# Kernel optimization log

Hardware: AMD Instinct MI355X
Metric: run time of the kernel (lower is better)

The kernel has to match this reference:

```python
import jax, jax.numpy as jnp
import numpy as np

B, T, C, H = 4, 2048, 1024, 16
HS = C // H  # head_size = 64
FF = 4 * C   # 4096
EPS = 1e-5


def _layernorm(x, g, b):
    mu = jnp.mean(x, axis=-1, keepdims=True)
    var = jnp.mean(jnp.square(x - mu), axis=-1, keepdims=True)
    return (x - mu) * jax.lax.rsqrt(var + EPS) * g + b


def setup_inputs() -> dict:
    key = jax.random.key(0)
    ks = jax.random.split(key, 12)
    s_in = 1.0 / np.sqrt(C)
    s_ff = 1.0 / np.sqrt(FF)
    return {
        "x": jax.random.normal(ks[0], (B, T, C), jnp.float32),
        # per-head projection weights stacked: [H, C, HS]
        "Wq": jax.random.normal(ks[1], (H, C, HS), jnp.float32) * s_in,
        "Wk": jax.random.normal(ks[2], (H, C, HS), jnp.float32) * s_in,
        "Wv": jax.random.normal(ks[3], (H, C, HS), jnp.float32) * s_in,
        "Wo": jax.random.normal(ks[4], (C, C), jnp.float32) * s_in,
        "bo": jnp.zeros((C,), jnp.float32),
        "g1": jnp.ones((C,), jnp.float32),
        "b1": jnp.zeros((C,), jnp.float32),
        "g2": jnp.ones((C,), jnp.float32),
        "b2": jnp.zeros((C,), jnp.float32),
        "W1": jax.random.normal(ks[5], (C, FF), jnp.float32) * s_in,
        "bf1": jnp.zeros((FF,), jnp.float32),
        "W2": jax.random.normal(ks[6], (FF, C), jnp.float32) * s_ff,
        "bf2": jnp.zeros((C,), jnp.float32),
    }


def reference(x, Wq, Wk, Wv, Wo, bo, g1, b1, g2, b2, W1, bf1, W2, bf2):
    # pre-norm
    h = _layernorm(x, g1, b1)                       # [B,T,C]
    q = jnp.einsum('btc,hcd->bhtd', h, Wq)          # [B,H,T,HS]
    k = jnp.einsum('btc,hcd->bhtd', h, Wk)
    v = jnp.einsum('btc,hcd->bhtd', h, Wv)
    w = jnp.einsum('bhtd,bhsd->bhts', q, k) * (HS ** -0.5)  # [B,H,T,S]
    mask = jnp.tril(jnp.ones((T, T), bool))          # causal tril
    w = jnp.where(mask[None, None], w, -jnp.inf)
    # NB: original code softmaxes over dim=1 of [B,T,T], i.e. the QUERY axis
    w = jax.nn.softmax(w, axis=-2)
    o = jnp.einsum('bhts,bhsd->bhtd', w, v)          # [B,H,T,HS]
    o = jnp.transpose(o, (0, 2, 1, 3)).reshape(B, T, C)  # concat heads
    x = x + o @ Wo + bo                              # residual 1 (dropout=0)
    f = _layernorm(x, g2, b2)
    ff = jax.nn.relu(f @ W1 + bf1) @ W2 + bf2        # FFN (dropout=0)
    return x + ff
```

## Files before the change

kernel.cpp:

```cpp
#include <hip/hip_runtime.h>


#define T_SEQ 2048
#define SCALE2 0.1803368801f

typedef __attribute__((ext_vector_type(8))) short short8;
typedef __attribute__((ext_vector_type(4))) float f32x4;

typedef __attribute__((address_space(1))) unsigned int g_u32;
typedef __attribute__((address_space(3))) unsigned int l_u32;

__device__ __forceinline__ unsigned short f2bf(float f) {
  union { float f; unsigned u; } x; x.f = f;
  unsigned r = (x.u + 0x7FFFu + ((x.u >> 16) & 1u)) >> 16;
  return (unsigned short)r;
}

__device__ __forceinline__ void g2lds16(const void* g, void* l) {
  __builtin_amdgcn_global_load_lds((g_u32*)g, (l_u32*)l, 16, 0, 0);
}

template <int EPI>
__global__ __launch_bounds__(256) void gemm_bt(
    const unsigned short* __restrict__ A, const unsigned short* __restrict__ Bt,
    int M, int N, int K,
    unsigned short* __restrict__ out16, float* __restrict__ outF,
    const float* __restrict__ bias, const float* __restrict__ resid) {
  __shared__ unsigned short ldsA[128 * 64];
  __shared__ unsigned short ldsB[128 * 64];
  const int tid = threadIdx.x;
  const int lane = tid & 63, wid = tid >> 6;
  const int wm = wid >> 1, wn = wid & 1;
  const int mBase = blockIdx.y * 128, nBase = blockIdx.x * 128;

  f32x4 acc[4][4];
#pragma unroll
  for (int i = 0; i < 4; ++i)
#pragma unroll
    for (int j = 0; j < 4; ++j)
#pragma unroll
      for (int e = 0; e < 4; ++e) acc[i][j][e] = 0.f;

  const int nKT = K >> 6;
  for (int kt = 0; kt < nKT; ++kt) {
    const int k0 = kt << 6;
#pragma unroll
    for (int it = 0; it < 4; ++it) {
      int g = it * 256 + wid * 64 + lane;
      int row = g >> 3, colL = g & 7;
      int col = colL ^ (row & 7);
      g2lds16(A + ((size_t)(mBase + row) * K + k0 + col * 8),
              &ldsA[(it * 256 + wid * 64) * 8]);
      g2lds16(Bt + ((size_t)(nBase + row) * K + k0 + col * 8),
              &ldsB[(it * 256 + wid * 64) * 8]);
    }
    __syncthreads();

    short8 af[4][2], bf[4][2];
#pragma unroll
    for (int fm = 0; fm < 4; ++fm)
#pragma unroll
      for (int ks = 0; ks < 2; ++ks) {
        int r = wm * 64 + fm * 16 + (lane & 15);
        int c = (ks * 4 + (lane >> 4)) ^ (r & 7);
        af[fm][ks] = *(const short8*)&ldsA[r * 64 + c * 8];
      }
#pragma unroll
    for (int fn = 0; fn < 4; ++fn)
#pragma unroll
      for (int ks = 0; ks < 2; ++ks) {
        int r = wn * 64 + fn * 16 + (lane & 15);
        int c = (ks * 4 + (lane >> 4)) ^ (r & 7);
        bf[fn][ks] = *(const short8*)&ldsB[r * 64 + c * 8];
      }
#pragma unroll
    for (int fm = 0; fm < 4; ++fm)
#pragma unroll
      for (int fn = 0; fn < 4; ++fn)
#pragma unroll
        for (int ks = 0; ks < 2; ++ks)
          acc[fm][fn] = __builtin_amdgcn_mfma_f32_16x16x32_bf16(
              af[fm][ks], bf[fn][ks], acc[fm][fn], 0, 0, 0);
    __syncthreads();
  }

#pragma unroll
  for (int fm = 0; fm < 4; ++fm)
#pragma unroll
    for (int fn = 0; fn < 4; ++fn) {
      int col = nBase + wn * 64 + fn * 16 + (lane & 15);
      int row0 = mBase + wm * 64 + fm * 16 + ((lane >> 4) << 2);
      if (EPI == 0) {
#pragma unroll
        for (int r = 0; r < 4; ++r)
          out16[(size_t)(row0 + r) * N + col] = f2bf(acc[fm][fn][r]);
      } else if (EPI == 1) {
        float bv = bias[col];
#pragma unroll
        for (int r = 0; r < 4; ++r) {
          size_t idx = (size_t)(row0 + r) * N + col;
          outF[idx] = acc[fm][fn][r] + bv + resid[idx];
        }
      } else {
        float bv = bias[col];
#pragma unroll
        for (int r = 0; r < 4; ++r)
          out16[(size_t)(row0 + r) * N + col] =
              f2bf(fmaxf(acc[fm][fn][r] + bv, 0.f));
      }
    }
}

__global__ __launch_bounds__(256) void ln_bf16(
    const float* __restrict__ x, const float* __restrict__ gw,
    const float* __restrict__ bw, unsigned short* __restrict__ out) {
  __shared__ float red[8];
  const int row = blockIdx.x, tid = threadIdx.x;
  const float4 v = ((const float4*)(x + (size_t)row * 1024))[tid];
  float s = v.x + v.y + v.z + v.w;
  float q = v.x * v.x + v.y * v.y + v.z * v.z + v.w * v.w;
#pragma unroll
  for (int off = 32; off >= 1; off >>= 1) {
    s += __shfl_down(s, off);
    q += __shfl_down(q, off);
  }
  const int lane = tid & 63, wid = tid >> 6;
  if (lane == 0) { red[wid] = s; red[4 + wid] = q; }
  __syncthreads();
  float S = red[0] + red[1] + red[2] + red[3];
  float Q = red[4] + red[5] + red[6] + red[7];
  float mu = S * (1.f / 1024.f);
  float var = Q * (1.f / 1024.f) - mu * mu;
  float rs = rsqrtf(var + 1e-5f);
  int c = tid * 4;
  ushort4 ov;
  ov.x = f2bf((v.x - mu) * rs * gw[c + 0] + bw[c + 0]);
  ov.y = f2bf((v.y - mu) * rs * gw[c + 1] + bw[c + 1]);
  ov.z = f2bf((v.z - mu) * rs * gw[c + 2] + bw[c + 2]);
  ov.w = f2bf((v.w - mu) * rs * gw[c + 3] + bw[c + 3]);
  *(ushort4*)&out[(size_t)row * 1024 + c] = ov;
}

__global__ __launch_bounds__(256) void pack_qkv(
    const float* __restrict__ Wq, const float* __restrict__ Wk,
    const float* __restrict__ Wv, unsigned short* __restrict__ out) {
  __shared__ float tile[64 * 65];
  const int tid = threadIdx.x;
  const float* W = (blockIdx.z == 0) ? Wq : (blockIdx.z == 1) ? Wk : Wv;
  const int h = blockIdx.y, r0 = blockIdx.x * 64;
#pragma unroll
  for (int it = 0; it < 4; ++it) {
    int e4 = it * 256 + tid;
    int r = e4 >> 4, c4 = e4 & 15;
    float4 v = *(const float4*)&W[((size_t)h * 1024 + r0 + r) * 64 + c4 * 4];
    tile[r * 65 + c4 * 4 + 0] = v.x;
    tile[r * 65 + c4 * 4 + 1] = v.y;
    tile[r * 65 + c4 * 4 + 2] = v.z;
    tile[r * 65 + c4 * 4 + 3] = v.w;
  }
  __syncthreads();
#pragma unroll
  for (int it = 0; it < 4; ++it) {
    int e4 = it * 256 + tid;
    int d = e4 >> 4, r4 = e4 & 15;
    ushort4 ov;
    ov.x = f2bf(tile[(r4 * 4 + 0) * 65 + d]);
    ov.y = f2bf(tile[(r4 * 4 + 1) * 65 + d]);
    ov.z = f2bf(tile[(r4 * 4 + 2) * 65 + d]);
    ov.w = f2bf(tile[(r4 * 4 + 3) * 65 + d]);
    *(ushort4*)&out[(size_t)(blockIdx.z * 1024 + h * 64 + d) * 1024 + r0 +
                    r4 * 4] = ov;
  }
}

__global__ __launch_bounds__(256) void transpose_cast(
    const float* __restrict__ in, unsigned short* __restrict__ out, int R,
    int C) {
  __shared__ float tile[64 * 65];
  const int tid = threadIdx.x;
  const int r0 = blockIdx.x * 64, c0 = blockIdx.y * 64;
#pragma unroll
  for (int it = 0; it < 4; ++it) {
    int e4 = it * 256 + tid;
    int r = e4 >> 4, c4 = e4 & 15;
    float4 v = *(const float4*)&in[(size_t)(r0 + r) * C + c0 + c4 * 4];
    tile[r * 65 + c4 * 4 + 0] = v.x;
    tile[r * 65 + c4 * 4 + 1] = v.y;
    tile[r * 65 + c4 * 4 + 2] = v.z;
    tile[r * 65 + c4 * 4 + 3] = v.w;
  }
  __syncthreads();
#pragma unroll
  for (int it = 0; it < 4; ++it) {
    int e4 = it * 256 + tid;
    int c = e4 >> 4, r4 = e4 & 15;
    ushort4 ov;
    ov.x = f2bf(tile[(r4 * 4 + 0) * 65 + c]);
    ov.y = f2bf(tile[(r4 * 4 + 1) * 65 + c]);
    ov.z = f2bf(tile[(r4 * 4 + 2) * 65 + c]);
    ov.w = f2bf(tile[(r4 * 4 + 3) * 65 + c]);
    *(ushort4*)&out[(size_t)(c0 + c) * R + r0 + r4 * 4] = ov;
  }
}

__global__ __launch_bounds__(256) void vtrans(
    const unsigned short* __restrict__ qkv, unsigned short* __restrict__ vT) {
  __shared__ unsigned short tile[64 * 66];
  const int tid = threadIdx.x;
  const int bh = blockIdx.y, b = bh >> 4, h = bh & 15;
  const int t0 = blockIdx.x * 64;
#pragma unroll
  for (int it = 0; it < 8; ++it) {
    int e2 = it * 256 + tid;
    int r = e2 >> 5, c2 = e2 & 31;
    unsigned v = *(const unsigned*)&qkv[(size_t)(b * T_SEQ + t0 + r) * 3072 +
                                        2048 + h * 64 + c2 * 2];
    *(unsigned*)&tile[r * 66 + c2 * 2] = v;
  }
  __syncthreads();
#pragma unroll
  for (int it = 0; it < 8; ++it) {
    int e2 = it * 256 + tid;
    int d = e2 >> 5, t2 = e2 & 31;
    unsigned short a = tile[(t2 * 2) * 66 + d];
    unsigned short bb = tile[(t2 * 2 + 1) * 66 + d];
    unsigned pk = (unsigned)a | ((unsigned)bb << 16);
    *(unsigned*)&vT[(size_t)(bh * 64 + d) * T_SEQ + t0 + t2 * 2] = pk;
  }
}

__global__ __launch_bounds__(256) void attn_stats(
    const unsigned short* __restrict__ qkv, float* __restrict__ linvOut) {
  __shared__ unsigned short qt[4][2][64 * 64];
  __shared__ float redL[4][2][64];
  const int tid = threadIdx.x, lane = tid & 63, w = tid >> 6;
  const int bh = blockIdx.y, b = bh >> 4, h = bh & 15;
  const int sx = blockIdx.x;
  const int sA = sx * 64, sB = (31 - sx) * 64;
  const int nT = 32 - sx;
  const int bDiag = 31 - 2 * sx;

  short8 kfA[4][2], kfB[4][2];
#pragma unroll
  for (int fn = 0; fn < 4; ++fn)
#pragma unroll
    for (int ks = 0; ks < 2; ++ks) {
      int d = 1024 + h * 64 + ks * 32 + ((lane >> 4) << 3);
      kfA[fn][ks] = *(const short8*)&qkv[(size_t)(b * T_SEQ + sA + fn * 16 +
                                                  (lane & 15)) * 3072 + d];
      kfB[fn][ks] = *(const short8*)&qkv[(size_t)(b * T_SEQ + sB + fn * 16 +
                                                  (lane & 15)) * 3072 + d];
    }
  float lA[4] = {0.f, 0.f, 0.f, 0.f}, lB[4] = {0.f, 0.f, 0.f, 0.f};

  auto stageQ = [&](int buf, int idx) {
    int t0 = sA + idx * 64;
#pragma unroll
    for (int it = 0; it < 8; ++it) {
      int g = it * 64 + lane;
      int row = g >> 3;
      int col = (g & 7) ^ (row & 7);
      g2lds16(qkv + ((size_t)(b * T_SEQ + t0 + row) * 3072 + h * 64 + col * 8),
              &qt[w][buf][it * 512]);
    }
  };

  auto accum = [&](const short8 (&af)[2], const short8 (&kf)[4][2],
                   float (&lacc)[4], int sBase, int t0, int mf, bool diag) {
    f32x4 sc[4];
#pragma unroll
    for (int fn = 0; fn < 4; ++fn)
#pragma unroll
      for (int e = 0; e < 4; ++e) sc[fn][e] = 0.f;
    __builtin_amdgcn_s_setprio(1);
#pragma unroll
    for (int fn = 0; fn < 4; ++fn)
#pragma unroll
      for (int ks = 0; ks < 2; ++ks)
        sc[fn] = __builtin_amdgcn_mfma_f32_16x16x32_bf16(af[ks], kf[fn][ks],
                                                         sc[fn], 0, 0, 0);
    __builtin_amdgcn_s_setprio(0);
    const int tRow = t0 + mf * 16 + ((lane >> 4) << 2);
    if (diag) {
#pragma unroll
      for (int fn = 0; fn < 4; ++fn) {
        int s = sBase + fn * 16 + (lane & 15);
#pragma unroll
        for (int r = 0; r < 4; ++r) {
          float e = exp2f(sc[fn][r] * SCALE2);
          lacc[fn] += (tRow + r >= s) ? e : 0.f;
        }
      }
    } else {
#pragma unroll
      for (int fn = 0; fn < 4; ++fn)
#pragma unroll
        for (int r = 0; r < 4; ++r) lacc[fn] += exp2f(sc[fn][r] * SCALE2);
    }
  };

  int idx = w, cur = 0;
  stageQ(0, idx);
  for (; idx < nT; idx += 4, cur ^= 1) {
    if (idx + 4 < nT) {
      stageQ(cur ^ 1, idx + 4);
      asm volatile("s_waitcnt vmcnt(8)" ::: "memory");
    } else {
      asm volatile("s_waitcnt vmcnt(0)" ::: "memory");
    }
    const int t0 = sA + idx * 64;
    const bool doB = idx >= bDiag;
#pragma unroll
    for (int mf = 0; mf < 4; ++mf) {
      short8 af[2];
#pragma unroll
      for (int ks = 0; ks < 2; ++ks) {
        int r = mf * 16 + (lane & 15);
        int c = (ks * 4 + (lane >> 4)) ^ (r & 7);
        af[ks] = *(const short8*)&qt[w][cur][r * 64 + c * 8];
      }
      accum(af, kfA, lA, sA, t0, mf, idx == 0);
      if (doB) accum(af, kfB, lB, sB, t0, mf, idx == bDiag);
    }
  }
#pragma unroll
  for (int fn = 0; fn < 4; ++fn) {
    lA[fn] += __shfl_down(lA[fn], 32);
    lA[fn] += __shfl_down(lA[fn], 16);
    lB[fn] += __shfl_down(lB[fn], 32);
    lB[fn] += __shfl_down(lB[fn], 16);
  }
  if (lane < 16) {
#pragma unroll
    for (int fn = 0; fn < 4; ++fn) {
      redL[w][0][fn * 16 + lane] = lA[fn];
      redL[w][1][fn * 16 + lane] = lB[fn];
    }
  }
  __syncthreads();
  if (tid < 128) {
    int which = tid >> 6;
    float l = redL[0][which][lane] + redL[1][which][lane] +
              redL[2][which][lane] + redL[3][which][lane];
    int sbase = (which == 0) ? sA : sB;
    linvOut[(size_t)bh * T_SEQ + sbase + lane] = 1.f / l;
  }
}

__global__ __launch_bounds__(256, 2) void attn_pv(
    const unsigned short* __restrict__ qkv, const unsigned short* __restrict__ vT,
    const float* __restrict__ linvIn, unsigned short* __restrict__ o) {
  __shared__ unsigned short kbuf[2][64 * 64];
  __shared__ unsigned short vbuf[2][64 * 64];
  __shared__ unsigned short pl[256 * 64];
  const int tid = threadIdx.x, lane = tid & 63, wid = tid >> 6;
  const int bh = blockIdx.y, b = bh >> 4, h = bh & 15;
  const int bx = blockIdx.x;
  const int tA = bx * 128, tB = (15 - bx) * 128;
  const int nSTA = 2 * bx + 2, nSTB = 32 - 2 * bx;

  short8 qfA[2][2], qfB[2][2];
#pragma unroll
  for (int mf = 0; mf < 2; ++mf)
#pragma unroll
    for (int ks = 0; ks < 2; ++ks) {
      int d = h * 64 + ks * 32 + ((lane >> 4) << 3);
      int rloc = wid * 32 + mf * 16 + (lane & 15);
      qfA[mf][ks] =
          *(const short8*)&qkv[(size_t)(b * T_SEQ + tA + rloc) * 3072 + d];
      qfB[mf][ks] =
          *(const short8*)&qkv[(size_t)(b * T_SEQ + tB + rloc) * 3072 + d];
    }
  f32x4 oaccA[2][4], oaccB[2][4];
#pragma unroll
  for (int i = 0; i < 2; ++i)
#pragma unroll
    for (int j = 0; j < 4; ++j)
#pragma unroll
      for (int e = 0; e < 4; ++e) { oaccA[i][j][e] = 0.f; oaccB[i][j][e] = 0.f; }

  auto stage = [&](int buf, int st) {
#pragma unroll
    for (int it = 0; it < 2; ++it) {
      int g = it * 256 + tid;
      int row = g >> 3, colL = g & 7;
      int col = colL ^ (row & 7);
      g2lds16(qkv + ((size_t)(b * T_SEQ + st * 64 + row) * 3072 + 1024 +
                     h * 64 + col * 8),
              &kbuf[buf][(it * 256 + wid * 64) * 8]);
      g2lds16(vT + ((size_t)(bh * 64 + row) * T_SEQ + st * 64 + col * 8),
              &vbuf[buf][(it * 256 + wid * 64) * 8]);
    }
  };

  auto qkstore = [&](const short8 (&qf)[2][2], int rowBase, int tBase, int s0,
                     float cc, bool maskNeeded, int cur) {
    f32x4 sc[2][4];
#pragma unroll
    for (int i = 0; i < 2; ++i)
#pragma unroll
      for (int j = 0; j < 4; ++j)
#pragma unroll
        for (int e = 0; e < 4; ++e) sc[i][j][e] = 0.f;
    __builtin_amdgcn_s_setprio(1);
#pragma unroll
    for (int fn = 0; fn < 4; ++fn)
#pragma unroll
      for (int ks = 0; ks < 2; ++ks) {
        int r = fn * 16 + (lane & 15);
        int c = (ks * 4 + (lane >> 4)) ^ (r & 7);
        short8 kfr = *(const short8*)&kbuf[cur][r * 64 + c * 8];
        sc[0][fn] = __builtin_amdgcn_mfma_f32_16x16x32_bf16(qf[0][ks], kfr,
                                                            sc[0][fn], 0, 0, 0);
        sc[1][fn] = __builtin_amdgcn_mfma_f32_16x16x32_bf16(qf[1][ks], kfr,
                                                            sc[1][fn], 0, 0, 0);
      }
    __builtin_amdgcn_s_setprio(0);
#pragma unroll
    for (int fn = 0; fn < 4; ++fn) {
      float ccf = __shfl(cc, fn * 16 + (lane & 15));
      int sg = s0 + fn * 16 + (lane & 15);
      int colb = (fn * 16 + (lane & 15)) * 2;
#pragma unroll
      for (int mf = 0; mf < 2; ++mf) {
        int rowB = rowBase + wid * 32 + mf * 16 + ((lane >> 4) << 2);
        int tRow = tBase + wid * 32 + mf * 16 + ((lane >> 4) << 2);
#pragma unroll
        for (int r = 0; r < 4; ++r) {
          float p = exp2f(fmaf(sc[mf][fn][r], SCALE2, ccf));
          if (maskNeeded) p = (tRow + r >= sg) ? p : 0.f;
          int row = rowB + r;
          int byteoff = row * 128 + (colb ^ ((row & 7) << 4));
          *(unsigned short*)((char*)pl + byteoff) = f2bf(p);
        }
      }
    }
  };

  stage(0, 0);
  int cur = 0;
  __syncthreads();

  for (int st = 0; st < nSTB; ++st) {
    const int s0 = st * 64;
    float lv = linvIn[(size_t)bh * T_SEQ + s0 + lane];
    float cc = __log2f(lv);
    const bool doA = st < nSTA;

    if (doA) qkstore(qfA, 0, tA, s0, cc, st >= nSTA - 2, cur);
    qkstore(qfB, 128, tB, s0, cc, st >= nSTB - 2, cur);
    __syncthreads();

    if (st + 1 < nSTB) stage(cur ^ 1, st + 1);

    __builtin_amdgcn_s_setprio(1);
#pragma unroll
    for (int ks = 0; ks < 2; ++ks) {
      short8 paA[2], paB[2];
#pragma unroll
      for (int mf = 0; mf < 2; ++mf) {
        int rowa = wid * 32 + mf * 16 + (lane & 15);
        int kb = ks * 64 + ((lane >> 4) << 4);
        paB[mf] = *(const short8*)((const char*)pl + (128 + rowa) * 128 +
                                   (kb ^ ((rowa & 7) << 4)));
        if (doA)
          paA[mf] = *(const short8*)((const char*)pl + rowa * 128 +
                                     (kb ^ ((rowa & 7) << 4)));
      }
#pragma unroll
      for (int df = 0; df < 4; ++df) {
        int r = df * 16 + (lane & 15);
        int c = (ks * 4 + (lane >> 4)) ^ (r & 7);
        short8 vb = *(const short8*)&vbuf[cur][r * 64 + c * 8];
        oaccB[0][df] = __builtin_amdgcn_mfma_f32_16x16x32_bf16(paB[0], vb,
                                                               oaccB[0][df], 0, 0, 0);
        oaccB[1][df] = __builtin_amdgcn_mfma_f32_16x16x32_bf16(paB[1], vb,
                                                               oaccB[1][df], 0, 0, 0);
        if (doA) {
          oaccA[0][df] = __builtin_amdgcn_mfma_f32_16x16x32_bf16(paA[0], vb,
                                                                 oaccA[0][df], 0, 0, 0);
          oaccA[1][df] = __builtin_amdgcn_mfma_f32_16x16x32_bf16(paA[1], vb,
                                                                 oaccA[1][df], 0, 0, 0);
        }
      }
    }
    __builtin_amdgcn_s_setprio(0);
    __syncthreads();
    cur ^= 1;
  }
#pragma unroll
  for (int mf = 0; mf < 2; ++mf)
#pragma unroll
    for (int df = 0; df < 4; ++df) {
      int d = h * 64 + df * 16 + (lane & 15);
      int ra = tA + wid * 32 + mf * 16 + ((lane >> 4) << 2);
      int rb = tB + wid * 32 + mf * 16 + ((lane >> 4) << 2);
#pragma unroll
      for (int r = 0; r < 4; ++r) {
        o[(size_t)(b * T_SEQ + ra + r) * 1024 + d] = f2bf(oaccA[mf][df][r]);
        o[(size_t)(b * T_SEQ + rb + r) * 1024 + d] = f2bf(oaccB[mf][df][r]);
      }
    }
}

extern "C" void kernel_launch(void* const* d_in, const int* in_sizes, int n_in,
                              void* d_out, int out_size, void* d_ws,
                              size_t ws_size, hipStream_t stream) {
  const float* x = (const float*)d_in[0];
  const float* Wq = (const float*)d_in[1];
  const float* Wk = (const float*)d_in[2];
  const float* Wv = (const float*)d_in[3];
  const float* Wo = (const float*)d_in[4];
  const float* bo = (const float*)d_in[5];
  const float* g1 = (const float*)d_in[6];
  const float* b1 = (const float*)d_in[7];
  const float* g2 = (const float*)d_in[8];
  const float* b2 = (const float*)d_in[9];
  const float* W1 = (const float*)d_in[10];
  const float* bf1 = (const float*)d_in[11];
  const float* W2 = (const float*)d_in[12];
  const float* bf2 = (const float*)d_in[13];
  float* out = (float*)d_out;

  char* ws = (char*)d_ws;
  size_t off = 0;
  auto alloc = [&](size_t bytes) {
    char* p = ws + off;
    off += (bytes + 255) & ~(size_t)255;
    return p;
  };
  unsigned short* Wqkv = (unsigned short*)alloc(3072ull * 1024 * 2);
  unsigned short* WoT = (unsigned short*)alloc(1024ull * 1024 * 2);
  unsigned short* W1T = (unsigned short*)alloc(4096ull * 1024 * 2);
  unsigned short* W2T = (unsigned short*)alloc(1024ull * 4096 * 2);
  unsigned short* hbuf = (unsigned short*)alloc(8192ull * 1024 * 2);
  char* regionE = alloc(8192ull * 3072 * 2 + 64ull * 64 * 2048 * 2);
  unsigned short* qkv = (unsigned short*)regionE;
  unsigned short* vT = (unsigned short*)(regionE + 8192ull * 3072 * 2);
  unsigned short* act = (unsigned short*)regionE;
  float* lbuf = (float*)alloc(64ull * 2048 * 4);
  float* x1 = (float*)alloc(8192ull * 1024 * 4);
  unsigned short* fbuf = (unsigned short*)alloc(8192ull * 1024 * 2);
  unsigned short* obuf = hbuf;

  (void)in_sizes; (void)n_in; (void)out_size; (void)ws_size;

  pack_qkv<<<dim3(16, 16, 3), 256, 0, stream>>>(Wq, Wk, Wv, Wqkv);
  transpose_cast<<<dim3(16, 16), 256, 0, stream>>>(Wo, WoT, 1024, 1024);
  transpose_cast<<<dim3(16, 64), 256, 0, stream>>>(W1, W1T, 1024, 4096);
  transpose_cast<<<dim3(64, 16), 256, 0, stream>>>(W2, W2T, 4096, 1024);
  ln_bf16<<<8192, 256, 0, stream>>>(x, g1, b1, hbuf);
  gemm_bt<0><<<dim3(24, 64), 256, 0, stream>>>(hbuf, Wqkv, 8192, 3072, 1024,
                                               qkv, nullptr, nullptr, nullptr);
  vtrans<<<dim3(32, 64), 256, 0, stream>>>(qkv, vT);
  attn_stats<<<dim3(16, 64), 256, 0, stream>>>(qkv, lbuf);
  attn_pv<<<dim3(8, 64), 256, 0, stream>>>(qkv, vT, lbuf, obuf);
  gemm_bt<1><<<dim3(8, 64), 256, 0, stream>>>(obuf, WoT, 8192, 1024, 1024,
                                              nullptr, x1, bo, x);
  ln_bf16<<<8192, 256, 0, stream>>>(x1, g2, b2, fbuf);
  gemm_bt<2><<<dim3(32, 64), 256, 0, stream>>>(fbuf, W1T, 8192, 4096, 1024, act,
                                               nullptr, bf1, nullptr);
  gemm_bt<1><<<dim3(8, 64), 256, 0, stream>>>(act, W2T, 8192, 1024, 4096,
                                              nullptr, out, bf2, x1);
}
```

Before: 471.7 us.

## Add 256x256 double-buffered GEMM, XCD swizzle, and fold softmax normalizer into V

Introduces a 512-thread 256x256-tile GEMM with double-buffered LDS staging (128KB dynamic shared) for the QKV and FFN1 projections, aiming to raise data reuse and overlap loads with MFMA. It adds an XCD-aware block swizzle and MFMA priority hints to the existing GEMM. It also moves the per-key softmax normalizer (query-axis softmax) into the V transpose by scaling V rows, which removes the per-tile log/shuffle/fma from the attention inner loop. Scaling V before bf16 rounding changes rounding slightly, and the large LDS footprint limits occupancy.

```diff
diff --git a/kernel.cpp b/kernel.cpp
--- a/kernel.cpp
+++ b/kernel.cpp
@@ -15,9 +15,117 @@
   unsigned r = (x.u + 0x7FFFu + ((x.u >> 16) & 1u)) >> 16;
   return (unsigned short)r;
 }
+__device__ __forceinline__ float bf2f(unsigned short u) {
+  union { unsigned u; float f; } x; x.u = (unsigned)u << 16;
+  return x.f;
+}
 
 __device__ __forceinline__ void g2lds16(const void* g, void* l) {
   __builtin_amdgcn_global_load_lds((g_u32*)g, (l_u32*)l, 16, 0, 0);
+}
+
+__device__ __forceinline__ int xcd_swz(int flat, int nwg) {
+  if ((nwg & 7) != 0) return flat;
+  return (flat & 7) * (nwg >> 3) + (flat >> 3);
+}
+
+template <int EPI>
+__global__ __launch_bounds__(512, 2) void gemm256(
+    const unsigned short* __restrict__ A, const unsigned short* __restrict__ Bt,
+    int M, int N, int K,
+    unsigned short* __restrict__ out16, const float* __restrict__ bias) {
+  extern __shared__ unsigned short lds[];
+  unsigned short* ldsA = lds;
+  unsigned short* ldsB = lds + 2 * 16384;
+  const int tid = threadIdx.x, lane = tid & 63, wid = tid >> 6;
+  const int wm = wid >> 2, wn = wid & 3;
+  const int nx = gridDim.x;
+  const int flat = blockIdx.y * nx + blockIdx.x;
+  const int swz = xcd_swz(flat, nx * gridDim.y);
+  const int mBase = (swz / nx) * 256, nBase = (swz % nx) * 256;
+
+  f32x4 acc[8][4];
+#pragma unroll
+  for (int i = 0; i < 8; ++i)
+#pragma unroll
+    for (int j = 0; j < 4; ++j)
+#pragma unroll
+      for (int e = 0; e < 4; ++e) acc[i][j][e] = 0.f;
+
+  auto stage = [&](int buf, int kt) {
+    const int k0 = kt << 6;
+#pragma unroll
+    for (int it = 0; it < 4; ++it) {
+      int g = it * 512 + tid;
+      int row = g >> 3, colL = g & 7;
+      int col = colL ^ (row & 7);
+      g2lds16(A + ((size_t)(mBase + row) * K + k0 + col * 8),
+              &ldsA[buf * 16384 + (it * 512 + wid * 64) * 8]);
+      g2lds16(Bt + ((size_t)(nBase + row) * K + k0 + col * 8),
+              &ldsB[buf * 16384 + (it * 512 + wid * 64) * 8]);
+    }
+  };
+
+  const int nKT = K >> 6;
+  stage(0, 0);
+  __syncthreads();
+  int cur = 0;
+  for (int kt = 0; kt < nKT; ++kt) {
+    if (kt + 1 < nKT) stage(cur ^ 1, kt + 1);
+
+    short8 bf[4][2];
+#pragma unroll
+    for (int fn = 0; fn < 4; ++fn)
+#pragma unroll
+      for (int ks = 0; ks < 2; ++ks) {
+        int r = wn * 64 + fn * 16 + (lane & 15);
+        int c = (ks * 4 + (lane >> 4)) ^ (r & 7);
+        bf[fn][ks] = *(const short8*)&ldsB[cur * 16384 + r * 64 + c * 8];
+      }
+#pragma unroll
+    for (int q = 0; q < 4; ++q) {
+      short8 af[2][2];
+#pragma unroll
+      for (int mf = 0; mf < 2; ++mf)
+#pragma unroll
+        for (int ks = 0; ks < 2; ++ks) {
+          int r = wm * 128 + q * 32 + mf * 16 + (lane & 15);
+          int c = (ks * 4 + (lane >> 4)) ^ (r & 7);
+          af[mf][ks] = *(const short8*)&ldsA[cur * 16384 + r * 64 + c * 8];
+        }
+      __builtin_amdgcn_s_setprio(1);
+#pragma unroll
+      for (int mf = 0; mf < 2; ++mf)
+#pragma unroll
+        for (int fn = 0; fn < 4; ++fn)
+#pragma unroll
+          for (int ks = 0; ks < 2; ++ks)
+            acc[q * 2 + mf][fn] = __builtin_amdgcn_mfma_f32_16x16x32_bf16(
+                af[mf][ks], bf[fn][ks], acc[q * 2 + mf][fn], 0, 0, 0);
+      __builtin_amdgcn_s_setprio(0);
+    }
+    __syncthreads();
+    cur ^= 1;
+  }
+
+#pragma unroll
+  for (int am = 0; am < 8; ++am)
+#pragma unroll
+    for (int fn = 0; fn < 4; ++fn) {
+      int col = nBase + wn * 64 + fn * 16 + (lane & 15);
+      int row0 = mBase + wm * 128 + am * 16 + ((lane >> 4) << 2);
+      if (EPI == 0) {
+#pragma unroll
+        for (int r = 0; r < 4; ++r)
+          out16[(size_t)(row0 + r) * N + col] = f2bf(acc[am][fn][r]);
+      } else {
+        float bv = bias[col];
+#pragma unroll
+        for (int r = 0; r < 4; ++r)
+          out16[(size_t)(row0 + r) * N + col] =
+              f2bf(fmaxf(acc[am][fn][r] + bv, 0.f));
+      }
+    }
 }
 
 template <int EPI>
@@ -31,7 +139,10 @@
   const int tid = threadIdx.x;
   const int lane = tid & 63, wid = tid >> 6;
   const int wm = wid >> 1, wn = wid & 1;
-  const int mBase = blockIdx.y * 128, nBase = blockIdx.x * 128;
+  const int nx = gridDim.x;
+  const int flat = blockIdx.y * nx + blockIdx.x;
+  const int swz = xcd_swz(flat, nx * gridDim.y);
+  const int mBase = (swz / nx) * 128, nBase = (swz % nx) * 128;
 
   f32x4 acc[4][4];
 #pragma unroll
@@ -73,6 +184,7 @@
         int c = (ks * 4 + (lane >> 4)) ^ (r & 7);
         bf[fn][ks] = *(const short8*)&ldsB[r * 64 + c * 8];
       }
+    __builtin_amdgcn_s_setprio(1);
 #pragma unroll
     for (int fm = 0; fm < 4; ++fm)
 #pragma unroll
@@ -81,6 +193,7 @@
         for (int ks = 0; ks < 2; ++ks)
           acc[fm][fn] = __builtin_amdgcn_mfma_f32_16x16x32_bf16(
               af[fm][ks], bf[fn][ks], acc[fm][fn], 0, 0, 0);
+    __builtin_amdgcn_s_setprio(0);
     __syncthreads();
   }
 
@@ -204,7 +317,8 @@
 }
 
 __global__ __launch_bounds__(256) void vtrans(
-    const unsigned short* __restrict__ qkv, unsigned short* __restrict__ vT) {
+    const unsigned short* __restrict__ qkv, const float* __restrict__ linv,
+    unsigned short* __restrict__ vT) {
   __shared__ unsigned short tile[64 * 66];
   const int tid = threadIdx.x;
   const int bh = blockIdx.y, b = bh >> 4, h = bh & 15;
@@ -215,7 +329,10 @@
     int r = e2 >> 5, c2 = e2 & 31;
     unsigned v = *(const unsigned*)&qkv[(size_t)(b * T_SEQ + t0 + r) * 3072 +
                                         2048 + h * 64 + c2 * 2];
-    *(unsigned*)&tile[r * 66 + c2 * 2] = v;
+    float li = linv[(size_t)bh * T_SEQ + t0 + r];
+    unsigned short lo = f2bf(bf2f((unsigned short)(v & 0xffff)) * li);
+    unsigned short hi = f2bf(bf2f((unsigned short)(v >> 16)) * li);
+    *(unsigned*)&tile[r * 66 + c2 * 2] = (unsigned)lo | ((unsigned)hi << 16);
   }
   __syncthreads();
 #pragma unroll
@@ -349,7 +466,7 @@
 
 __global__ __launch_bounds__(256, 2) void attn_pv(
     const unsigned short* __restrict__ qkv, const unsigned short* __restrict__ vT,
-    const float* __restrict__ linvIn, unsigned short* __restrict__ o) {
+    unsigned short* __restrict__ o) {
   __shared__ unsigned short kbuf[2][64 * 64];
   __shared__ unsigned short vbuf[2][64 * 64];
   __shared__ unsigned short pl[256 * 64];
@@ -394,7 +511,7 @@
   };
 
   auto qkstore = [&](const short8 (&qf)[2][2], int rowBase, int tBase, int s0,
-                     float cc, bool maskNeeded, int cur) {
+                     bool maskNeeded, int cur) {
     f32x4 sc[2][4];
 #pragma unroll
     for (int i = 0; i < 2; ++i)
@@ -418,7 +535,6 @@
     __builtin_amdgcn_s_setprio(0);
 #pragma unroll
     for (int fn = 0; fn < 4; ++fn) {
-      float ccf = __shfl(cc, fn * 16 + (lane & 15));
       int sg = s0 + fn * 16 + (lane & 15);
       int colb = (fn * 16 + (lane & 15)) * 2;
 #pragma unroll
@@ -427,7 +543,7 @@
         int tRow = tBase + wid * 32 + mf * 16 + ((lane >> 4) << 2);
 #pragma unroll
         for (int r = 0; r < 4; ++r) {
-          float p = exp2f(fmaf(sc[mf][fn][r], SCALE2, ccf));
+          float p = exp2f(sc[mf][fn][r] * SCALE2);
           if (maskNeeded) p = (tRow + r >= sg) ? p : 0.f;
           int row = rowB + r;
           int byteoff = row * 128 + (colb ^ ((row & 7) << 4));
@@ -443,12 +559,10 @@
 
   for (int st = 0; st < nSTB; ++st) {
     const int s0 = st * 64;
-    float lv = linvIn[(size_t)bh * T_SEQ + s0 + lane];
-    float cc = __log2f(lv);
     const bool doA = st < nSTA;
 
-    if (doA) qkstore(qfA, 0, tA, s0, cc, st >= nSTA - 2, cur);
-    qkstore(qfB, 128, tB, s0, cc, st >= nSTB - 2, cur);
+    if (doA) qkstore(qfA, 0, tA, s0, st >= nSTA - 2, cur);
+    qkstore(qfB, 128, tB, s0, st >= nSTB - 2, cur);
     __syncthreads();
 
     if (st + 1 < nSTB) stage(cur ^ 1, st + 1);
@@ -550,16 +664,16 @@
   transpose_cast<<<dim3(16, 64), 256, 0, stream>>>(W1, W1T, 1024, 4096);
   transpose_cast<<<dim3(64, 16), 256, 0, stream>>>(W2, W2T, 4096, 1024);
   ln_bf16<<<8192, 256, 0, stream>>>(x, g1, b1, hbuf);
-  gemm_bt<0><<<dim3(24, 64), 256, 0, stream>>>(hbuf, Wqkv, 8192, 3072, 1024,
-                                               qkv, nullptr, nullptr, nullptr);
-  vtrans<<<dim3(32, 64), 256, 0, stream>>>(qkv, vT);
+  gemm256<0><<<dim3(12, 32), 512, 131072, stream>>>(hbuf, Wqkv, 8192, 3072,
+                                                    1024, qkv, nullptr);
   attn_stats<<<dim3(16, 64), 256, 0, stream>>>(qkv, lbuf);
-  attn_pv<<<dim3(8, 64), 256, 0, stream>>>(qkv, vT, lbuf, obuf);
+  vtrans<<<dim3(32, 64), 256, 0, stream>>>(qkv, lbuf, vT);
+  attn_pv<<<dim3(8, 64), 256, 0, stream>>>(qkv, vT, obuf);
   gemm_bt<1><<<dim3(8, 64), 256, 0, stream>>>(obuf, WoT, 8192, 1024, 1024,
                                               nullptr, x1, bo, x);
   ln_bf16<<<8192, 256, 0, stream>>>(x1, g2, b2, fbuf);
-  gemm_bt<2><<<dim3(32, 64), 256, 0, stream>>>(fbuf, W1T, 8192, 4096, 1024, act,
-                                               nullptr, bf1, nullptr);
+  gemm256<2><<<dim3(16, 32), 512, 131072, stream>>>(fbuf, W1T, 8192, 4096,
+                                                    1024, act, bf1);
   gemm_bt<1><<<dim3(8, 64), 256, 0, stream>>>(act, W2T, 8192, 1024, 4096,
                                               nullptr, out, bf2, x1);
 }
```

Result: faster. 435.8 us (-7.6%).
